# Performance work log

Hardware: AMD Instinct MI355X
Metric: run time of the kernel (lower is better)

## Reference

```python
import jax, jax.numpy as jnp
import numpy as np
from jax import lax

EPS_BN = 1e-5
EPS_LN = 1e-5
IMG = 240
BETA = 1.0

def l2norm(x, axis=-1):
    n = jnp.linalg.norm(x, axis=axis, keepdims=True)
    return x / jnp.maximum(n, 1e-12)

def bn2d(x, g, b):
    # training-mode BatchNorm2d: stats over (B,H,W), biased variance
    m = x.mean(axis=(0, 2, 3), keepdims=True)
    v = x.var(axis=(0, 2, 3), keepdims=True)
    return g[None, :, None, None] * (x - m) * lax.rsqrt(v + EPS_BN) + b[None, :, None, None]

def conv2d(x, w):
    return lax.conv_general_dilated(x, w, (1, 1), 'SAME', dimension_numbers=('NCHW', 'OIHW', 'NCHW'))

def convT2x2(x, w, b):
    # ConvTranspose2d k=2 s=2 pad=0; torch weight layout (C_in, C_out, 2, 2)
    B, C, H, W = x.shape
    O = w.shape[1]
    y = jnp.einsum('bchw,copq->bohpwq', x, w).reshape(B, O, 2 * H, 2 * W)
    return y + b[None, :, None, None]

def layernorm(x, g, b):
    m = x.mean(-1, keepdims=True)
    v = x.var(-1, keepdims=True)
    return g * (x - m) * lax.rsqrt(v + EPS_LN) + b

def setup_inputs() -> dict:
    key = jax.random.key(0)
    ks = jax.random.split(key, 12)
    L, B, K, N, D = 3, 16, 8, 256, 768
    H, MID = 128, 64
    inp = {
        'query': jax.random.normal(ks[0], (L, B, N, D), jnp.float32),
        'prompt': jax.random.normal(ks[1], (L, B, K, N, D), jnp.float32),
        'sharebn_g': jnp.ones((L, D)), 'sharebn_b': jnp.zeros((L, D)),
        'lw1': 0.02 * jax.random.normal(ks[2], (L, H, D, 3, 3)),
        'lbn1g': jnp.ones((L, H)), 'lbn1b': jnp.zeros((L, H)),
        'lwt1': 0.05 * jax.random.normal(ks[3], (L, H, H, 2, 2)), 'lbt1': jnp.zeros((L, H)),
        'lw2': 0.02 * jax.random.normal(ks[4], (L, MID, H, 3, 3)),
        'lbn2g': jnp.ones((L, MID)), 'lbn2b': jnp.zeros((L, MID)),
        'lwt2': 0.05 * jax.random.normal(ks[5], (L, MID, MID, 2, 2)), 'lbt2': jnp.zeros((L, MID)),
        'lw3': 0.05 * jax.random.normal(ks[6], (L, 2, MID, 1, 1)), 'lb3': jnp.zeros((L, 2)),
        'pool_logits': jnp.zeros((L, 2)),
        'mw1': 0.02 * jax.random.normal(ks[7], (L, H, D)),
        'mlng': jnp.ones((L, H)), 'mlnb': jnp.zeros((L, H)),
        'mw2': 0.05 * jax.random.normal(ks[8], (L, 2, H)), 'mb2': jnp.zeros((L, 2)),
    }
    return inp

def _layer(q, pf, p):
    # q: [B,N,D], pf: [B,M,D]
    B, N, D = q.shape
    g = int(N ** 0.5)
    qn = l2norm(q)
    pn = l2norm(pf)
    sim = jnp.einsum('bnc,bmc->bnm', qn, pn)              # [B,N,M]
    max_cos = sim.max(axis=-1)
    idx = sim.argmax(axis=-1)                              # [B,N]
    aligned = jnp.take_along_axis(pf, idx[:, :, None], axis=1)  # [B,N,D]
    residual = 0.5 * (1.0 - max_cos)
    an = l2norm(aligned)
    ctx = qn + BETA * jnp.abs(qn - an)                     # [B,N,D]
    cmap = ctx.transpose(0, 2, 1).reshape(B, D, g, g)
    cmap = bn2d(cmap, p['sbg'], p['sbb'])
    # local conv head
    x = jax.nn.relu(bn2d(conv2d(cmap, p['w1']), p['bn1g'], p['bn1b']))
    x = convT2x2(x, p['wt1'], p['bt1'])
    x = jax.nn.relu(bn2d(conv2d(x, p['w2']), p['bn2g'], p['bn2b']))
    x = convT2x2(x, p['wt2'], p['bt2'])
    raw = conv2d(x, p['w3']) + p['b3'][None, :, None, None]   # [B,2,4g,4g]
    # adaptive_avg_pool2d 4g -> g (exact 4x4 blocks)
    pl2c = raw.reshape(B, 2, g, 4, g, 4).mean(axis=(3, 5))    # [B,2,g,g]
    ps2c = jax.nn.softmax(pl2c, axis=1)
    patch_logits = (pl2c[:, 1] - pl2c[:, 0]).reshape(B, -1)
    patch_scores = ps2c[:, 1].reshape(B, -1)
    local_logits = jax.image.resize(raw, (B, 2, IMG, IMG), method='bilinear')
    # global head (GAP/GMP fusion over context map features)
    cf = cmap.reshape(B, D, N)
    gap = cf.mean(axis=-1)
    gmp = cf.max(axis=-1)
    pw = jax.nn.softmax(p['pl'])
    pooled = pw[0] * gap + pw[1] * gmp                     # [B,D]
    h = jax.nn.relu(layernorm(pooled @ p['mw1'].T, p['lng'], p['lnb']))
    logits2 = h @ p['mw2'].T + p['mb2']
    glogit = logits2[:, 1] - logits2[:, 0]
    return residual, patch_scores, patch_logits, glogit, local_logits, pw, idx, aligned

def reference(query, prompt, sharebn_g, sharebn_b, lw1, lbn1g, lbn1b, lwt1, lbt1,
              lw2, lbn2g, lbn2b, lwt2, lbt2, lw3, lb3, pool_logits,
              mw1, mlng, mlnb, mw2, mb2):
    L, B = query.shape[0], query.shape[1]
    outs = []
    for l in range(L):
        pf = prompt[l].reshape(B, -1, prompt.shape[-1])
        p = dict(sbg=sharebn_g[l], sbb=sharebn_b[l], w1=lw1[l], bn1g=lbn1g[l], bn1b=lbn1b[l],
                 wt1=lwt1[l], bt1=lbt1[l], w2=lw2[l], bn2g=lbn2g[l], bn2b=lbn2b[l],
                 wt2=lwt2[l], bt2=lbt2[l], w3=lw3[l], b3=lb3[l], pl=pool_logits[l],
                 mw1=mw1[l], lng=mlng[l], lnb=mlnb[l], mw2=mw2[l], mb2=mb2[l])
        outs.append(_layer(query[l], pf, p))
    stacked = tuple(jnp.stack([o[i] for o in outs]) for i in range(8))
    return stacked
```

## Files before the change

### kernel.cpp

```cpp
#include <hip/hip_runtime.h>
#include <hip/hip_bf16.h>
#include <math.h>

#define LLY 3
#define BB 16
#define NNQ 256
#define DD 768
#define MMP 2048
#define HH 128
#define MD 64
#define IMGSZ 240
#define LBTOT (LLY*BB)

#define OFF_INVQ 0
#define OFF_INVP (OFF_INVQ + LLY*BB*NNQ)
#define OFF_CMAP (OFF_INVP + LLY*BB*MMP)
#define OFF_BNSH (OFF_CMAP + LLY*BB*DD*NNQ)
#define OFF_X1   (OFF_BNSH + 2*LLY*DD)
#define OFF_BN1  (OFF_X1 + LLY*BB*HH*256)
#define OFF_T1   (OFF_BN1 + 2*LLY*HH)
#define OFF_X2   (OFF_T1 + LLY*BB*HH*1024)
#define OFF_BN2  (OFF_X2 + LLY*BB*MD*1024)
#define OFF_T2   (OFF_BN2 + 2*LLY*MD)
#define OFF_RAW3 (OFF_T2 + LLY*BB*MD*4096)
#define WS_FLOATS (OFF_RAW3 + LLY*BB*2*4096)
#define T1BSH (LBTOT*1024*HH)
#define SQH   (LBTOT*NNQ*DD)
#define OFF_C1P (OFF_T2 + 4718592)
#define OFF_C2P (OFF_T2 + 3256320)
#define OFF_PGL OFF_X1
#define X1B_SH 0
#define WT1B_SH 1600000

#define O_RES 0
#define O_PSC (O_RES + LLY*BB*NNQ)
#define O_PLG (O_PSC + LLY*BB*NNQ)
#define O_GLG (O_PLG + LLY*BB*NNQ)
#define O_LOC (O_GLG + LLY*BB)
#define O_PW  (O_LOC + LLY*BB*2*IMGSZ*IMGSZ)
#define O_IDX (O_PW + LLY*2)
#define O_ALN (O_IDX + LLY*BB*NNQ)

typedef __attribute__((ext_vector_type(8))) short bf16x8;
typedef __attribute__((ext_vector_type(4))) float f32x4;

__device__ __forceinline__ unsigned short f2bf(float f) {
    __hip_bfloat16 h = __float2bfloat16(f);
    unsigned short u;
    __builtin_memcpy(&u, &h, sizeof(u));
    return u;
}
__device__ __forceinline__ float bf2f(unsigned short h) {
    return __uint_as_float(((unsigned int)h) << 16);
}

__device__ __forceinline__ float blockReduceSum(float v, float* sm) {
    for (int o = 32; o; o >>= 1) v += __shfl_down(v, o, 64);
    __syncthreads();
    if ((threadIdx.x & 63) == 0) sm[threadIdx.x >> 6] = v;
    __syncthreads();
    return sm[0] + sm[1] + sm[2] + sm[3];
}

__global__ __launch_bounds__(192) void knormq(const float* __restrict__ query,
                                              float* __restrict__ ws) {
    __shared__ float sm[3];
    int row = blockIdx.x;
    int t = threadIdx.x;
    float4 v = *(const float4*)(query + (size_t)row * DD + t * 4);
    float ss = v.x * v.x + v.y * v.y + v.z * v.z + v.w * v.w;
    for (int o = 32; o; o >>= 1) ss += __shfl_down(ss, o, 64);
    if ((t & 63) == 0) sm[t >> 6] = ss;
    __syncthreads();
    ss = sm[0] + sm[1] + sm[2];
    float iv = 1.0f / fmaxf(sqrtf(ss), 1e-12f);
    if (t == 0) ws[OFF_INVQ + row] = iv;
    unsigned short* qh = (unsigned short*)(ws + OFF_T2);
    unsigned short* ql = qh + SQH;
    float e[4] = {v.x * iv, v.y * iv, v.z * iv, v.w * iv};
    unsigned int hp[2], lp[2];
    #pragma unroll
    for (int j = 0; j < 2; j++) {
        unsigned short h0 = f2bf(e[2*j]), h1 = f2bf(e[2*j+1]);
        unsigned short l0 = f2bf(e[2*j] - bf2f(h0)), l1 = f2bf(e[2*j+1] - bf2f(h1));
        hp[j] = (unsigned int)h0 | ((unsigned int)h1 << 16);
        lp[j] = (unsigned int)l0 | ((unsigned int)l1 << 16);
    }
    *(uint2*)(qh + (size_t)row * DD + t * 4) = make_uint2(hp[0], hp[1]);
    *(uint2*)(ql + (size_t)row * DD + t * 4) = make_uint2(lp[0], lp[1]);
}

__global__ __launch_bounds__(512) void ksimm(const float* __restrict__ prompt, float* __restrict__ ws) {
    __shared__ __align__(16) unsigned short Ah[128][40];
    __shared__ __align__(16) unsigned short Al[128][40];
    __shared__ __align__(16) unsigned short Bh[256][40];
    __shared__ __align__(16) unsigned short Bl[256][40];
    __shared__ float invL[128];
    int bid = blockIdx.x;
    int mt = bid & 15;
    int lb = bid >> 4;
    int t = threadIdx.x;
    int lane = t & 63, wave = t >> 6;
    int wm = wave >> 2, wn = wave & 3;
    int fr = lane & 15, fq = lane >> 4;
    const unsigned short* qh = (const unsigned short*)(ws + OFF_T2);
    const unsigned short* ql = qh + SQH;
    const float* pbase = prompt + (size_t)lb * MMP * DD + (size_t)(mt * 128) * DD;

    float ssq[2] = {0.f, 0.f};

    f32x4 acc[4][4];
    #pragma unroll
    for (int mi = 0; mi < 4; mi++)
        #pragma unroll
        for (int ni = 0; ni < 4; ni++) acc[mi][ni] = (f32x4){0.f, 0.f, 0.f, 0.f};

    for (int kc = 0; kc < DD; kc += 32) {
        __syncthreads();
        #pragma unroll
        for (int i = 0; i < 2; i++) {
            int f = t + i * 512;
            int row = f >> 3, c4 = f & 7;
            float4 v = *(const float4*)(pbase + (size_t)row * DD + kc + c4 * 4);
            ssq[i] += v.x * v.x + v.y * v.y + v.z * v.z + v.w * v.w;
            unsigned short h0 = f2bf(v.x), h1 = f2bf(v.y), h2 = f2bf(v.z), h3 = f2bf(v.w);
            unsigned short l0 = f2bf(v.x - bf2f(h0)), l1 = f2bf(v.y - bf2f(h1));
            unsigned short l2 = f2bf(v.z - bf2f(h2)), l3 = f2bf(v.w - bf2f(h3));
            uint2 hp = make_uint2((unsigned int)h0 | ((unsigned int)h1 << 16),
                                  (unsigned int)h2 | ((unsigned int)h3 << 16));
            uint2 lp = make_uint2((unsigned int)l0 | ((unsigned int)l1 << 16),
                                  (unsigned int)l2 | ((unsigned int)l3 << 16));
            *(uint2*)&Ah[row][c4 * 4] = hp;
            *(uint2*)&Al[row][c4 * 4] = lp;
        }
        #pragma unroll
        for (int i = 0; i < 2; i++) {
            int f = t + i * 512;
            int row = f >> 2, sg = f & 3;
            size_t go = (size_t)(lb * NNQ + row) * DD + kc + sg * 8;
            *(uint4*)&Bh[row][sg * 8] = *(const uint4*)(qh + go);
            *(uint4*)&Bl[row][sg * 8] = *(const uint4*)(ql + go);
        }
        __syncthreads();
        bf16x8 ah[4], al4[4], bh[4], bl4[4];
        #pragma unroll
        for (int mi = 0; mi < 4; mi++) {
            ah[mi]  = *(const bf16x8*)&Ah[wm * 64 + mi * 16 + fr][fq * 8];
            al4[mi] = *(const bf16x8*)&Al[wm * 64 + mi * 16 + fr][fq * 8];
        }
        #pragma unroll
        for (int ni = 0; ni < 4; ni++) {
            bh[ni]  = *(const bf16x8*)&Bh[wn * 64 + ni * 16 + fr][fq * 8];
            bl4[ni] = *(const bf16x8*)&Bl[wn * 64 + ni * 16 + fr][fq * 8];
        }
        #pragma unroll
        for (int mi = 0; mi < 4; mi++)
            #pragma unroll
            for (int ni = 0; ni < 4; ni++) {
                acc[mi][ni] = __builtin_amdgcn_mfma_f32_16x16x32_bf16(ah[mi],  bh[ni],  acc[mi][ni], 0, 0, 0);
                acc[mi][ni] = __builtin_amdgcn_mfma_f32_16x16x32_bf16(ah[mi],  bl4[ni], acc[mi][ni], 0, 0, 0);
                acc[mi][ni] = __builtin_amdgcn_mfma_f32_16x16x32_bf16(al4[mi], bh[ni],  acc[mi][ni], 0, 0, 0);
            }
    }
    #pragma unroll
    for (int i = 0; i < 2; i++) {
        float s = ssq[i];
        s += __shfl_xor(s, 1, 64);
        s += __shfl_xor(s, 2, 64);
        s += __shfl_xor(s, 4, 64);
        if ((t & 7) == 0) {
            int row = (t >> 3) + 64 * i;
            float iv = 1.0f / fmaxf(sqrtf(s), 1e-12f);
            invL[row] = iv;
            ws[OFF_INVP + lb * MMP + mt * 128 + row] = iv;
        }
    }
    __syncthreads();
    float* bestv = ws + OFF_X1;
    float* besti = ws + OFF_X1 + (size_t)LBTOT * NNQ * 32;
    #pragma unroll
    for (int ni = 0; ni < 4; ni++) {
        float bv = -1e30f; int bi = 0;
        #pragma unroll
        for (int mi = 0; mi < 4; mi++)
            #pragma unroll
            for (int rr = 0; rr < 4; rr++) {
                int lm = wm * 64 + mi * 16 + fq * 4 + rr;
                float s = acc[mi][ni][rr] * invL[lm];
                int m = mt * 128 + lm;
                if (s > bv) { bv = s; bi = m; }
            }
        #pragma unroll
        for (int o = 16; o <= 32; o <<= 1) {
            float ov = __shfl_xor(bv, o, 64);
            int oi = __shfl_xor(bi, o, 64);
            if (ov > bv || (ov == bv && oi < bi)) { bv = ov; bi = oi; }
        }
        if (fq == 0) {
            int q = wn * 64 + ni * 16 + fr;
            size_t slot = (size_t)(lb * NNQ + q) * 32 + wm * 16 + mt;
            bestv[slot] = bv;
            besti[slot] = (float)bi;
        }
    }
}

__global__ __launch_bounds__(256) void kpost(const float* __restrict__ query,
                                             const float* __restrict__ prompt,
                                             float* __restrict__ ws,
                                             float* __restrict__ out) {
    __shared__ float red_v[16];
    __shared__ int   red_i[16];
    __shared__ float Lctx[DD * 17];
    int bid = blockIdx.x;
    int nt = bid & 15;
    int lb = bid >> 4;
    int t = threadIdx.x;
    const float* bestv = ws + OFF_X1;
    const float* besti = ws + OFF_X1 + (size_t)LBTOT * NNQ * 32;
    if (t < 16) {
        int q = nt * 16 + t;
        const float* bv = bestv + (size_t)(lb * NNQ + q) * 32;
        const float* bi = besti + (size_t)(lb * NNQ + q) * 32;
        float best = -1e30f; int bidx2 = 0;
        for (int mtt = 0; mtt < 16; mtt++)
            #pragma unroll
            for (int wm = 0; wm < 2; wm++) {
                float v = bv[wm * 16 + mtt];
                if (v > best) { best = v; bidx2 = (int)bi[wm * 16 + mtt]; }
            }
        red_v[t] = best; red_i[t] = bidx2;
        out[O_RES + lb * NNQ + q] = 0.5f * (1.0f - best);
        out[O_IDX + lb * NNQ + q] = (float)bidx2;
    }
    __syncthreads();
    const float* qbase = query + (size_t)(lb * NNQ + nt * 16) * DD;
    const float* pbase = prompt + (size_t)lb * MMP * DD;
    const float* invq = ws + OFF_INVQ + lb * NNQ + nt * 16;
    const float* invp = ws + OFF_INVP + lb * MMP;
    int c = t & 15;
    int nn = t >> 4;
    int gn = nt * 16 + nn;
    int midx = red_i[nn];
    float ip = invp[midx];
    float iq = invq[nn];
    const float* prow = pbase + (size_t)midx * DD;
    const float* qrow = qbase + (size_t)nn * DD;
    float* aln = out + O_ALN + (size_t)(lb * NNQ + gn) * DD;
    for (int jj = 0; jj < DD / 16; jj++) {
        int d = c + jj * 16;
        float pvr = prow[d];
        float qv = qrow[d] * iq;
        float av = pvr * ip;
        float cx = qv + fabsf(qv - av);
        aln[d] = pvr;
        Lctx[d * 17 + nn] = cx;
    }
    __syncthreads();
    float* cm = ws + OFF_CMAP + (size_t)lb * DD * NNQ + nt * 16;
    int nl = t & 15, dd = t >> 4;
    for (int jj = 0; jj < DD / 16; jj++) {
        int d = jj * 16 + dd;
        cm[(size_t)d * NNQ + nl] = Lctx[d * 17 + nl];
    }
}

__global__ __launch_bounds__(256) void kbnstats(const float* __restrict__ x, int C, int SP,
                                                const float* __restrict__ g,
                                                const float* __restrict__ b,
                                                float* __restrict__ outSB) {
    __shared__ float sm[4];
    int bid = blockIdx.x;
    int c = bid % C;
    int l = bid / C;
    int t = threadIdx.x;
    float s = 0.f, sq = 0.f;
    for (int bb2 = 0; bb2 < BB; ++bb2) {
        const float* p = x + ((size_t)(l * BB + bb2) * C + c) * SP;
        for (int i = t; i < SP; i += 256) { float v = p[i]; s += v; sq += v * v; }
    }
    s = blockReduceSum(s, sm);
    sq = blockReduceSum(sq, sm);
    if (t == 0) {
        float inv = 1.0f / (float)(BB * SP);
        float m = s * inv;
        float var = sq * inv - m * m;
        float sc = g[l * C + c] * rsqrtf(var + 1e-5f);
        float bo = b[l * C + c] - m * sc;
        outSB[l * C + c] = sc;
        outSB[LLY * C + l * C + c] = bo;
    }
}

__global__ __launch_bounds__(256) void kw1cvt(const float* __restrict__ lw1, float* __restrict__ ws) {
    unsigned short* w1B = (unsigned short*)(ws + OFF_X2);
    int bid = blockIdx.x;
    int l = bid / HH, co = bid % HH;
    int t = threadIdx.x;
    for (int c0 = 0; c0 < DD; c0 += 256) {
        int ci = c0 + t;
        const float* src = lw1 + ((size_t)(l * HH + co) * DD + ci) * 9;
        #pragma unroll
        for (int tap = 0; tap < 9; tap++) {
            w1B[((size_t)((l * 9 + tap) * HH + co)) * DD + ci] = f2bf(src[tap]);
        }
    }
}

__global__ __launch_bounds__(256) void kbn1cvt(float* __restrict__ ws) {
    __shared__ float Ld[64][65];
    unsigned short* cmT = (unsigned short*)(ws + OFF_T2);
    int bid = blockIdx.x;
    int nt = bid & 3;
    int r = bid >> 2;
    int ct = r % 12;
    int lb = r / 12;
    int l = lb >> 4;
    int t = threadIdx.x;
    const float* cmap = ws + OFF_CMAP + (size_t)lb * DD * NNQ;
    const float* bns = ws + OFF_BNSH + l * DD;
    const float* bnb = ws + OFF_BNSH + LLY * DD + l * DD;
    #pragma unroll
    for (int i = 0; i < 4; i++) {
        int f = t + i * 256;
        int row = f >> 4, c4 = f & 15;
        int ci = ct * 64 + row;
        float4 v = *(const float4*)(cmap + (size_t)ci * NNQ + nt * 64 + c4 * 4);
        float s = bns[ci], bo = bnb[ci];
        Ld[row][c4*4+0] = v.x * s + bo; Ld[row][c4*4+1] = v.y * s + bo;
        Ld[row][c4*4+2] = v.z * s + bo; Ld[row][c4*4+3] = v.w * s + bo;
    }
    __syncthreads();
    #pragma unroll
    for (int i = 0; i < 2; i++) {
        int f = t + i * 256;
        int row = f >> 3, seg = f & 7;
        unsigned int pk[4];
        #pragma unroll
        for (int e = 0; e < 4; e++) {
            unsigned int lo = f2bf(Ld[seg * 8 + 2 * e][row]);
            unsigned int hi = f2bf(Ld[seg * 8 + 2 * e + 1][row]);
            pk[e] = lo | (hi << 16);
        }
        uint4 o = make_uint4(pk[0], pk[1], pk[2], pk[3]);
        *(uint4*)(cmT + ((size_t)(lb * NNQ + nt * 64 + row)) * DD + ct * 64 + seg * 8) = o;
    }
}

__global__ __launch_bounds__(256) void kconv1m(float* __restrict__ ws) {
    __shared__ __align__(16) unsigned short Ab[128][72];
    __shared__ __align__(16) unsigned short Bb[128][72];
    int bid = blockIdx.x;
    int s = bid % 6;
    int ntile = (bid / 6) & 1;
    int lb = bid / 12;
    int l = lb >> 4;
    int t = threadIdx.x;
    int lane = t & 63;
    int wave = t >> 6;
    int wr = wave >> 1, wc = wave & 1;
    int fr = lane & 15, fq = lane >> 4;
    const unsigned short* w1B = (const unsigned short*)(ws + OFF_X2);
    const unsigned short* cmT = (const unsigned short*)(ws + OFF_T2);

    f32x4 acc[4][4];
    #pragma unroll
    for (int mi = 0; mi < 4; mi++)
        #pragma unroll
        for (int ni = 0; ni < 4; ni++) acc[mi][ni] = (f32x4){0.f, 0.f, 0.f, 0.f};

    for (int g = s * 18; g < s * 18 + 18; ++g) {
        int tap = g / 12;
        int kc = (g % 12) * 64;
        int dy = tap / 3 - 1, dx = tap % 3 - 1;
        const unsigned short* wpl = w1B + (size_t)((l * 9 + tap) * HH) * DD;
        __syncthreads();
        #pragma unroll
        for (int i = 0; i < 4; i++) {
            int f = t + i * 256;
            int row = f >> 3, seg = f & 7;
            uint4 v = *(const uint4*)(wpl + (size_t)row * DD + kc + seg * 8);
            *(uint4*)&Ab[row][seg * 8] = v;
        }
        #pragma unroll
        for (int i = 0; i < 4; i++) {
            int f = t + i * 256;
            int row = f >> 3, seg = f & 7;
            int n = ntile * 128 + row;
            int y = (n >> 4) + dy, x = (n & 15) + dx;
            bool ok = ((unsigned)y < 16u) && ((unsigned)x < 16u);
            uint4 v = make_uint4(0u, 0u, 0u, 0u);
            if (ok) v = *(const uint4*)(cmT + ((size_t)(lb * NNQ + y * 16 + x)) * DD + kc + seg * 8);
            *(uint4*)&Bb[row][seg * 8] = v;
        }
        __syncthreads();
        #pragma unroll
        for (int kk = 0; kk < 64; kk += 32) {
            bf16x8 af[4], bfv[4];
            #pragma unroll
            for (int mi = 0; mi < 4; mi++)
                af[mi] = *(const bf16x8*)&Ab[wr * 64 + mi * 16 + fr][kk + fq * 8];
            #pragma unroll
            for (int ni = 0; ni < 4; ni++)
                bfv[ni] = *(const bf16x8*)&Bb[wc * 64 + ni * 16 + fr][kk + fq * 8];
            #pragma unroll
            for (int mi = 0; mi < 4; mi++)
                #pragma unroll
                for (int ni = 0; ni < 4; ni++)
                    acc[mi][ni] = __builtin_amdgcn_mfma_f32_16x16x32_bf16(af[mi], bfv[ni], acc[mi][ni], 0, 0, 0);
        }
    }
    float* dst = (s == 5) ? (ws + OFF_X1 + (size_t)lb * HH * 256)
                          : (ws + OFF_C1P + (size_t)(s * LBTOT + lb) * (HH * 256));
    #pragma unroll
    for (int mi = 0; mi < 4; mi++) {
        #pragma unroll
        for (int ni = 0; ni < 4; ni++) {
            int gn = ntile * 128 + wc * 64 + ni * 16 + fr;
            #pragma unroll
            for (int rr = 0; rr < 4; rr++) {
                int co = wr * 64 + mi * 16 + fq * 4 + rr;
                dst[(size_t)co * 256 + gn] = acc[mi][ni][rr];
            }
        }
    }
}

__global__ __launch_bounds__(256) void kc1red(float* __restrict__ ws) {
    size_t i = ((size_t)blockIdx.x * 256 + threadIdx.x) * 8;
    float4 a0 = *(float4*)(ws + OFF_X1 + i);
    float4 a1 = *(float4*)(ws + OFF_X1 + i + 4);
    #pragma unroll
    for (int s = 0; s < 5; s++) {
        const float* p = ws + OFF_C1P + (size_t)s * (LBTOT * HH * 256) + i;
        float4 b0 = *(const float4*)p;
        float4 b1 = *(const float4*)(p + 4);
        a0.x += b0.x; a0.y += b0.y; a0.z += b0.z; a0.w += b0.w;
        a1.x += b1.x; a1.y += b1.y; a1.z += b1.z; a1.w += b1.w;
    }
    *(float4*)(ws + OFF_X1 + i) = a0;
    *(float4*)(ws + OFF_X1 + i + 4) = a1;
}

__global__ __launch_bounds__(256) void kxcvt(const float* __restrict__ x,
                                             const float* __restrict__ sbsb,
                                             unsigned short* __restrict__ xb,
                                             int CI, int SPIN, int nT, int cT) {
    __shared__ float Ld[64][65];
    int bid = blockIdx.x;
    int nt = bid % nT;
    int r = bid / nT;
    int ct = r % cT;
    int lb = r / cT;
    int l = lb >> 4;
    int t = threadIdx.x;
    const float* sc = sbsb + l * CI;
    const float* bo = sbsb + LLY * CI + l * CI;
    #pragma unroll
    for (int i = 0; i < 4; i++) {
        int f = t + i * 256;
        int row = f >> 4, c4 = f & 15;
        int ci = ct * 64 + row;
        float4 v = *(const float4*)(x + ((size_t)lb * CI + ci) * SPIN + nt * 64 + c4 * 4);
        float s = sc[ci], b_ = bo[ci];
        Ld[row][c4*4+0] = fmaxf(v.x * s + b_, 0.f);
        Ld[row][c4*4+1] = fmaxf(v.y * s + b_, 0.f);
        Ld[row][c4*4+2] = fmaxf(v.z * s + b_, 0.f);
        Ld[row][c4*4+3] = fmaxf(v.w * s + b_, 0.f);
    }
    __syncthreads();
    int segs = CI >> 3;
    for (int f = t; f < 64 * segs; f += 256) {
        int row = f / segs, seg = f % segs;
        int sl = seg - ct * 8;
        if (sl < 0 || sl >= 8) continue;
        unsigned int pk[4];
        #pragma unroll
        for (int e = 0; e < 4; e++) {
            unsigned int lo = f2bf(Ld[sl * 8 + 2 * e][row]);
            unsigned int hi = f2bf(Ld[sl * 8 + 2 * e + 1][row]);
            pk[e] = lo | (hi << 16);
        }
        uint4 o = make_uint4(pk[0], pk[1], pk[2], pk[3]);
        *(uint4*)(xb + ((size_t)lb * SPIN + nt * 64 + row) * CI + ct * 64 + sl * 8) = o;
    }
}

__global__ __launch_bounds__(128) void kwtcvt(const float* __restrict__ lwt,
                                              unsigned short* __restrict__ dst,
                                              int CI, int CO) {
    int bid = blockIdx.x;
    int l = bid / CO, co = bid % CO;
    int t = threadIdx.x;
    if (t < CI) {
        const float* src = lwt + (((size_t)(l * CI + t) * CO + co) * 4);
        #pragma unroll
        for (int pq = 0; pq < 4; pq++) {
            dst[((size_t)((l * 4 + pq) * CO + co)) * CI + t] = f2bf(src[pq]);
        }
    }
}

__global__ __launch_bounds__(256) void kconvTm(const unsigned short* __restrict__ xb,
                                               const unsigned short* __restrict__ wtb,
                                               const float* __restrict__ bt,
                                               float* __restrict__ xout,
                                               int CI, int CO, int gsh, int nTiles, int coTiles) {
    __shared__ __align__(16) unsigned short Ab[64][72];
    __shared__ __align__(16) unsigned short Bb[256][72];
    int bid = blockIdx.x;
    int ntile = bid % nTiles;
    int r = bid / nTiles;
    int cot = r % coTiles; r /= coTiles;
    int pq = r & 3;
    int lb = r >> 2;
    int l = lb >> 4;
    int SPIN = 1 << (2 * gsh);
    int t = threadIdx.x, lane = t & 63, wave = t >> 6;
    int fr = lane & 15, fq = lane >> 4;

    f32x4 acc[4][4];
    #pragma unroll
    for (int mi = 0; mi < 4; mi++)
        #pragma unroll
        for (int ni = 0; ni < 4; ni++) acc[mi][ni] = (f32x4){0.f, 0.f, 0.f, 0.f};

    for (int kc = 0; kc < CI; kc += 64) {
        __syncthreads();
        #pragma unroll
        for (int i = 0; i < 2; i++) {
            int f = t + i * 256;
            int row = f >> 3, seg = f & 7;
            *(uint4*)&Ab[row][seg * 8] =
                *(const uint4*)(wtb + ((size_t)((l * 4 + pq) * CO + cot * 64 + row)) * CI + kc + seg * 8);
        }
        #pragma unroll
        for (int i = 0; i < 8; i++) {
            int f = t + i * 256;
            int row = f >> 3, seg = f & 7;
            *(uint4*)&Bb[row][seg * 8] =
                *(const uint4*)(xb + ((size_t)lb * SPIN + ntile * 256 + row) * CI + kc + seg * 8);
        }
        __syncthreads();
        #pragma unroll
        for (int kk = 0; kk < 64; kk += 32) {
            bf16x8 af[4], bfv[4];
            #pragma unroll
            for (int mi = 0; mi < 4; mi++)
                af[mi] = *(const bf16x8*)&Ab[mi * 16 + fr][kk + fq * 8];
            #pragma unroll
            for (int ni = 0; ni < 4; ni++)
                bfv[ni] = *(const bf16x8*)&Bb[wave * 64 + ni * 16 + fr][kk + fq * 8];
            #pragma unroll
            for (int mi = 0; mi < 4; mi++)
                #pragma unroll
                for (int ni = 0; ni < 4; ni++)
                    acc[mi][ni] = __builtin_amdgcn_mfma_f32_16x16x32_bf16(af[mi], bfv[ni], acc[mi][ni], 0, 0, 0);
        }
    }
    int p = pq >> 1, q = pq & 1;
    int GIN = 1 << gsh;
    #pragma unroll
    for (int mi = 0; mi < 4; mi++) {
        #pragma unroll
        for (int rr = 0; rr < 4; rr++) {
            int co = cot * 64 + mi * 16 + fq * 4 + rr;
            float bias = bt[l * CO + co];
            float* orow = xout + ((size_t)(lb * CO + co)) * (4 * SPIN);
            #pragma unroll
            for (int ni = 0; ni < 4; ni++) {
                int n = ntile * 256 + wave * 64 + ni * 16 + fr;
                int h = n >> gsh, w = n & (GIN - 1);
                orow[(2 * h + p) * (2 * GIN) + 2 * w + q] = acc[mi][ni][rr] + bias;
            }
        }
    }
}

__global__ __launch_bounds__(256) void kconvT2f(const unsigned short* __restrict__ xb,
                                                const unsigned short* __restrict__ wtb,
                                                const float* __restrict__ bt,
                                                const float* __restrict__ lw3,
                                                const float* __restrict__ lb3,
                                                float* __restrict__ ws) {
    __shared__ __align__(16) unsigned short Ab[64][72];
    __shared__ __align__(16) unsigned short Bb[256][72];
    __shared__ float w3s[2][64];
    int bid = blockIdx.x;
    int ntile = bid & 3;
    int r = bid >> 2;
    int pq = r & 3;
    int lb = r >> 2;
    int l = lb >> 4;
    const int CI = MD, CO = MD, gsh = 5;
    int SPIN = 1 << (2 * gsh);
    int t = threadIdx.x, lane = t & 63, wave = t >> 6;
    int fr = lane & 15, fq = lane >> 4;
    if (t < 128) w3s[t >> 6][t & 63] = lw3[(size_t)(l * 2 + (t >> 6)) * MD + (t & 63)];

    f32x4 acc[4][4];
    #pragma unroll
    for (int mi = 0; mi < 4; mi++)
        #pragma unroll
        for (int ni = 0; ni < 4; ni++) acc[mi][ni] = (f32x4){0.f, 0.f, 0.f, 0.f};

    __syncthreads();
    #pragma unroll
    for (int i = 0; i < 2; i++) {
        int f = t + i * 256;
        int row = f >> 3, seg = f & 7;
        *(uint4*)&Ab[row][seg * 8] =
            *(const uint4*)(wtb + ((size_t)((l * 4 + pq) * CO + row)) * CI + seg * 8);
    }
    #pragma unroll
    for (int i = 0; i < 8; i++) {
        int f = t + i * 256;
        int row = f >> 3, seg = f & 7;
        *(uint4*)&Bb[row][seg * 8] =
            *(const uint4*)(xb + ((size_t)lb * SPIN + ntile * 256 + row) * CI + seg * 8);
    }
    __syncthreads();
    #pragma unroll
    for (int kk = 0; kk < 64; kk += 32) {
        bf16x8 af[4], bfv[4];
        #pragma unroll
        for (int mi = 0; mi < 4; mi++)
            af[mi] = *(const bf16x8*)&Ab[mi * 16 + fr][kk + fq * 8];
        #pragma unroll
        for (int ni = 0; ni < 4; ni++)
            bfv[ni] = *(const bf16x8*)&Bb[wave * 64 + ni * 16 + fr][kk + fq * 8];
        #pragma unroll
        for (int mi = 0; mi < 4; mi++)
            #pragma unroll
            for (int ni = 0; ni < 4; ni++)
                acc[mi][ni] = __builtin_amdgcn_mfma_f32_16x16x32_bf16(af[mi], bfv[ni], acc[mi][ni], 0, 0, 0);
    }
    float s0[4] = {0.f, 0.f, 0.f, 0.f};
    float s1[4] = {0.f, 0.f, 0.f, 0.f};
    #pragma unroll
    for (int mi = 0; mi < 4; mi++) {
        #pragma unroll
        for (int rr = 0; rr < 4; rr++) {
            int co = mi * 16 + fq * 4 + rr;
            float bias = bt[l * CO + co];
            float w0 = w3s[0][co], w1 = w3s[1][co];
            #pragma unroll
            for (int ni = 0; ni < 4; ni++) {
                float val = acc[mi][ni][rr] + bias;
                s0[ni] += w0 * val;
                s1[ni] += w1 * val;
            }
        }
    }
    #pragma unroll
    for (int ni = 0; ni < 4; ni++) {
        s0[ni] += __shfl_xor(s0[ni], 16, 64); s0[ni] += __shfl_xor(s0[ni], 32, 64);
        s1[ni] += __shfl_xor(s1[ni], 16, 64); s1[ni] += __shfl_xor(s1[ni], 32, 64);
    }
    if (fq == 0) {
        int p = pq >> 1, q = pq & 1;
        float* r3 = ws + OFF_RAW3 + (size_t)lb * 2 * 4096;
        float b30 = lb3[l * 2], b31 = lb3[l * 2 + 1];
        #pragma unroll
        for (int ni = 0; ni < 4; ni++) {
            int n = ntile * 256 + wave * 64 + ni * 16 + fr;
            int h = n >> 5, w = n & 31;
            int opix = (2 * h + p) * 64 + 2 * w + q;
            r3[opix] = s0[ni] + b30;
            r3[4096 + opix] = s1[ni] + b31;
        }
    }
}

__global__ __launch_bounds__(256) void kt1cvt(float* __restrict__ ws) {
    __shared__ float Ld[64][65];
    unsigned short* t1B = (unsigned short*)(ws + OFF_T2);
    int bid = blockIdx.x;
    int ntile = bid & 15;
    int r = bid >> 4;
    int ct = r & 1;
    int lb = r >> 1;
    int t = threadIdx.x;
    const float* t1p = ws + OFF_T1 + (size_t)lb * HH * 1024;
    #pragma unroll
    for (int i = 0; i < 4; i++) {
        int f = t + i * 256;
        int row = f >> 4, c4 = f & 15;
        float4 v = *(const float4*)(t1p + (size_t)(ct * 64 + row) * 1024 + ntile * 64 + c4 * 4);
        *(float4*)&Ld[row][c4 * 4] = v;
    }
    __syncthreads();
    #pragma unroll
    for (int i = 0; i < 2; i++) {
        int f = t + i * 256;
        int row = f >> 3, seg = f & 7;
        unsigned int pk[4];
        #pragma unroll
        for (int e = 0; e < 4; e++) {
            unsigned int lo = f2bf(Ld[seg * 8 + 2 * e][row]);
            unsigned int hi = f2bf(Ld[seg * 8 + 2 * e + 1][row]);
            pk[e] = lo | (hi << 16);
        }
        uint4 o = make_uint4(pk[0], pk[1], pk[2], pk[3]);
        *(uint4*)(t1B + ((size_t)(lb * 1024 + ntile * 64 + row)) * HH + ct * 64 + seg * 8) = o;
    }
}

__global__ __launch_bounds__(256) void kw2cvt(const float* __restrict__ lw2, float* __restrict__ ws) {
    unsigned short* w2B = (unsigned short*)(ws + OFF_T2) + T1BSH;
    int bid = blockIdx.x;
    int l = bid / MD, co = bid % MD;
    int t = threadIdx.x;
    if (t < HH) {
        int ci = t;
        const float* src = lw2 + ((size_t)(l * MD + co) * HH + ci) * 9;
        #pragma unroll
        for (int tap = 0; tap < 9; tap++) {
            w2B[((size_t)((l * 9 + tap) * MD + co)) * HH + ci] = f2bf(src[tap]);
        }
    }
}

__global__ __launch_bounds__(256) void kconv2m(float* __restrict__ ws) {
    __shared__ __align__(16) unsigned short Ab[64][72];
    __shared__ __align__(16) unsigned short Bb[256][72];
    int bid = blockIdx.x;
    int s = bid & 1;
    int ntile = (bid >> 1) & 3;
    int lb = bid >> 3;
    int l = lb >> 4;
    int t = threadIdx.x;
    int lane = t & 63;
    int wave = t >> 6;
    int fr = lane & 15, fq = lane >> 4;
    const unsigned short* t1B = (const unsigned short*)(ws + OFF_T2);
    const unsigned short* w2B = (const unsigned short*)(ws + OFF_T2) + T1BSH;

    f32x4 acc[4][4];
    #pragma unroll
    for (int mi = 0; mi < 4; mi++)
        #pragma unroll
        for (int ni = 0; ni < 4; ni++) acc[mi][ni] = (f32x4){0.f, 0.f, 0.f, 0.f};

    for (int g = s * 9; g < s * 9 + 9; ++g) {
        int tap = g >> 1;
        int kc = (g & 1) * 64;
        int dy = tap / 3 - 1, dx = tap % 3 - 1;
        const unsigned short* wpl = w2B + (size_t)((l * 9 + tap) * MD) * HH;
        __syncthreads();
        #pragma unroll
        for (int i = 0; i < 2; i++) {
            int f = t + i * 256;
            int row = f >> 3, seg = f & 7;
            uint4 v = *(const uint4*)(wpl + (size_t)row * HH + kc + seg * 8);
            *(uint4*)&Ab[row][seg * 8] = v;
        }
        #pragma unroll
        for (int i = 0; i < 8; i++) {
            int f = t + i * 256;
            int row = f >> 3, seg = f & 7;
            int n = ntile * 256 + row;
            int y = (n >> 5) + dy, x = (n & 31) + dx;
            bool ok = ((unsigned)y < 32u) && ((unsigned)x < 32u);
            uint4 v = make_uint4(0u, 0u, 0u, 0u);
            if (ok) v = *(const uint4*)(t1B + ((size_t)(lb * 1024 + y * 32 + x)) * HH + kc + seg * 8);
            *(uint4*)&Bb[row][seg * 8] = v;
        }
        __syncthreads();
        #pragma unroll
        for (int kk = 0; kk < 64; kk += 32) {
            bf16x8 af[4], bfv[4];
            #pragma unroll
            for (int mi = 0; mi < 4; mi++)
                af[mi] = *(const bf16x8*)&Ab[mi * 16 + fr][kk + fq * 8];
            #pragma unroll
            for (int ni = 0; ni < 4; ni++)
                bfv[ni] = *(const bf16x8*)&Bb[wave * 64 + ni * 16 + fr][kk + fq * 8];
            #pragma unroll
            for (int mi = 0; mi < 4; mi++)
                #pragma unroll
                for (int ni = 0; ni < 4; ni++)
                    acc[mi][ni] = __builtin_amdgcn_mfma_f32_16x16x32_bf16(af[mi], bfv[ni], acc[mi][ni], 0, 0, 0);
        }
    }
    float* dst = (s == 1) ? (ws + OFF_X2 + (size_t)lb * MD * 1024)
                          : (ws + OFF_C2P + (size_t)lb * MD * 1024);
    #pragma unroll
    for (int mi = 0; mi < 4; mi++) {
        #pragma unroll
        for (int ni = 0; ni < 4; ni++) {
            int gn = ntile * 256 + wave * 64 + ni * 16 + fr;
            #pragma unroll
            for (int rr = 0; rr < 4; rr++) {
                int co = mi * 16 + fq * 4 + rr;
                dst[(size_t)co * 1024 + gn] = acc[mi][ni][rr];
            }
        }
    }
}

__global__ __launch_bounds__(256) void kc2red(float* __restrict__ ws) {
    size_t i = ((size_t)blockIdx.x * 256 + threadIdx.x) * 8;
    float4 a0 = *(float4*)(ws + OFF_X2 + i);
    float4 a1 = *(float4*)(ws + OFF_X2 + i + 4);
    const float* p = ws + OFF_C2P + i;
    float4 b0 = *(const float4*)p;
    float4 b1 = *(const float4*)(p + 4);
    a0.x += b0.x; a0.y += b0.y; a0.z += b0.z; a0.w += b0.w;
    a1.x += b1.x; a1.y += b1.y; a1.z += b1.z; a1.w += b1.w;
    *(float4*)(ws + OFF_X2 + i) = a0;
    *(float4*)(ws + OFF_X2 + i + 4) = a1;
}

__global__ __launch_bounds__(256) void kpool(const float* __restrict__ ws, float* __restrict__ out) {
    int lb = blockIdx.x;
    int t = threadIdx.x;
    int gy = t >> 4, gx = t & 15;
    const float* r3 = ws + OFF_RAW3 + (size_t)lb * 2 * 4096;
    float pl[2];
    #pragma unroll
    for (int ch = 0; ch < 2; ch++) {
        const float* basep = r3 + ch * 4096;
        float s = 0.f;
        #pragma unroll
        for (int dy = 0; dy < 4; dy++)
            #pragma unroll
            for (int dx = 0; dx < 4; dx++)
                s += basep[(gy * 4 + dy) * 64 + gx * 4 + dx];
        pl[ch] = s * (1.f / 16.f);
    }
    out[O_PLG + lb * NNQ + t] = pl[1] - pl[0];
    out[O_PSC + lb * NNQ + t] = 1.f / (1.f + expf(pl[0] - pl[1]));
}

__global__ __launch_bounds__(256) void kresize(const float* __restrict__ ws, float* __restrict__ out) {
    int id = blockIdx.x * 256 + threadIdx.x;
    int ox = id % IMGSZ;
    int tmp = id / IMGSZ;
    int oy = tmp % IMGSZ;
    int tmp2 = tmp / IMGSZ;
    int ch = tmp2 & 1;
    int lb = tmp2 >> 1;
    const float S = 64.f / 240.f;
    float xs = fminf(fmaxf((ox + 0.5f) * S - 0.5f, 0.f), 63.f);
    float ys = fminf(fmaxf((oy + 0.5f) * S - 0.5f, 0.f), 63.f);
    int x0 = (int)xs, y0 = (int)ys;
    float fx = xs - x0, fy = ys - y0;
    int x1 = min(x0 + 1, 63), y1 = min(y0 + 1, 63);
    const float* basep = ws + OFF_RAW3 + (size_t)(lb * 2 + ch) * 4096;
    float v00 = basep[y0 * 64 + x0], v01 = basep[y0 * 64 + x1];
    float v10 = basep[y1 * 64 + x0], v11 = basep[y1 * 64 + x1];
    float v = (1.f - fy) * ((1.f - fx) * v00 + fx * v01) + fy * ((1.f - fx) * v10 + fx * v11);
    out[O_LOC + id] = v;
}

__global__ __launch_bounds__(256) void kgap(float* __restrict__ ws,
                                            const float* __restrict__ pool_logits) {
    int bid = blockIdx.x;
    int dchunk = bid % 12;
    int lb = bid / 12;
    int l = lb >> 4;
    int t = threadIdx.x;
    int r = t >> 2, p = t & 3;
    int d = dchunk * 64 + r;
    const float* row = ws + OFF_CMAP + (size_t)lb * DD * NNQ + (size_t)d * NNQ + p * 64;
    float s = 0.f, mx = -1e30f, mn = 1e30f;
    #pragma unroll
    for (int i = 0; i < 16; i++) {
        float4 v = *(const float4*)(row + i * 4);
        s += v.x + v.y + v.z + v.w;
        mx = fmaxf(mx, fmaxf(fmaxf(v.x, v.y), fmaxf(v.z, v.w)));
        mn = fminf(mn, fminf(fminf(v.x, v.y), fminf(v.z, v.w)));
    }
    s += __shfl_xor(s, 1, 64); s += __shfl_xor(s, 2, 64);
    mx = fmaxf(mx, __shfl_xor(mx, 1, 64)); mx = fmaxf(mx, __shfl_xor(mx, 2, 64));
    mn = fminf(mn, __shfl_xor(mn, 1, 64)); mn = fminf(mn, __shfl_xor(mn, 2, 64));
    if (p == 0) {
        float p0 = pool_logits[l * 2], p1 = pool_logits[l * 2 + 1];
        float mxp = fmaxf(p0, p1);
        float e0 = expf(p0 - mxp), e1 = expf(p1 - mxp);
        float pw0 = e0 / (e0 + e1), pw1 = e1 / (e0 + e1);
        const float* bns = ws + OFF_BNSH + l * DD;
        const float* bnb = ws + OFF_BNSH + LLY * DD + l * DD;
        float scv = bns[d], bov = bnb[d];
        float gap = scv * (s * (1.f / NNQ)) + bov;
        float gmp = (scv >= 0.f) ? (scv * mx + bov) : (scv * mn + bov);
        ws[OFF_PGL + lb * DD + d] = pw0 * gap + pw1 * gmp;
    }
}

__global__ __launch_bounds__(256) void kglob2(const float* __restrict__ ws,
                                              const float* __restrict__ pool_logits,
                                              const float* __restrict__ mw1,
                                              const float* __restrict__ mlng,
                                              const float* __restrict__ mlnb,
                                              const float* __restrict__ mw2,
                                              const float* __restrict__ mb2,
                                              float* __restrict__ out) {
    __shared__ float pooled[DD];
    __shared__ float zbuf[HH];
    __shared__ float hbuf[HH];
    __shared__ float sm[4];
    int lb = blockIdx.x;
    int l = lb >> 4;
    int b = lb & 15;
    int t = threadIdx.x;
    float p0 = pool_logits[l * 2], p1 = pool_logits[l * 2 + 1];
    float mx = fmaxf(p0, p1);
    float e0 = expf(p0 - mx), e1 = expf(p1 - mx);
    float pw0 = e0 / (e0 + e1), pw1 = e1 / (e0 + e1);
    if (b == 0 && t < 2) out[O_PW + l * 2 + t] = (t == 0) ? pw0 : pw1;

    for (int d = t; d < DD; d += 256) pooled[d] = ws[OFF_PGL + lb * DD + d];
    __syncthreads();
    if (t < HH) {
        const float* wrow = mw1 + (size_t)(l * HH + t) * DD;
        float a = 0.f;
        for (int d2 = 0; d2 < DD; d2++) a += pooled[d2] * wrow[d2];
        zbuf[t] = a;
    }
    __syncthreads();
    float zv = (t < HH) ? zbuf[t] : 0.f;
    float s1r = blockReduceSum(zv, sm);
    float s2r = blockReduceSum(zv * zv, sm);
    float mean = s1r * (1.f / HH);
    float var = s2r * (1.f / HH) - mean * mean;
    float rstd = rsqrtf(var + 1e-5f);
    if (t < HH) {
        float h = (zbuf[t] - mean) * rstd * mlng[l * HH + t] + mlnb[l * HH + t];
        hbuf[t] = fmaxf(h, 0.f);
    }
    __syncthreads();
    float hv = (t < HH) ? hbuf[t] : 0.f;
    float w0v = (t < HH) ? mw2[(size_t)(l * 2 + 0) * HH + t] : 0.f;
    float w1v = (t < HH) ? mw2[(size_t)(l * 2 + 1) * HH + t] : 0.f;
    float s0 = blockReduceSum(hv * w0v, sm);
    float s1 = blockReduceSum(hv * w1v, sm);
    if (t == 0) out[O_GLG + lb] = (s1 + mb2[l * 2 + 1]) - (s0 + mb2[l * 2]);
}

extern "C" void kernel_launch(void* const* d_in, const int* in_sizes, int n_in,
                              void* d_out, int out_size, void* d_ws, size_t ws_size,
                              hipStream_t stream) {
    const float* query      = (const float*)d_in[0];
    const float* prompt     = (const float*)d_in[1];
    const float* sharebn_g  = (const float*)d_in[2];
    const float* sharebn_b  = (const float*)d_in[3];
    const float* lw1        = (const float*)d_in[4];
    const float* lbn1g      = (const float*)d_in[5];
    const float* lbn1b      = (const float*)d_in[6];
    const float* lwt1       = (const float*)d_in[7];
    const float* lbt1       = (const float*)d_in[8];
    const float* lw2        = (const float*)d_in[9];
    const float* lbn2g      = (const float*)d_in[10];
    const float* lbn2b      = (const float*)d_in[11];
    const float* lwt2       = (const float*)d_in[12];
    const float* lbt2       = (const float*)d_in[13];
    const float* lw3        = (const float*)d_in[14];
    const float* lb3        = (const float*)d_in[15];
    const float* pool_logits= (const float*)d_in[16];
    const float* mw1        = (const float*)d_in[17];
    const float* mlng       = (const float*)d_in[18];
    const float* mlnb       = (const float*)d_in[19];
    const float* mw2        = (const float*)d_in[20];
    const float* mb2        = (const float*)d_in[21];
    float* out = (float*)d_out;
    float* ws = (float*)d_ws;

    hipLaunchKernelGGL(knormq, dim3(LLY*BB*NNQ), dim3(192), 0, stream, query, ws);
    hipLaunchKernelGGL(ksimm, dim3(LBTOT*16), dim3(512), 0, stream, prompt, ws);
    hipLaunchKernelGGL(kpost, dim3(LBTOT*16), dim3(256), 0, stream, query, prompt, ws, out);
    hipLaunchKernelGGL(kbnstats, dim3(LLY*DD), dim3(256), 0, stream,
                       ws + OFF_CMAP, DD, NNQ, sharebn_g, sharebn_b, ws + OFF_BNSH);
    hipLaunchKernelGGL(kw1cvt, dim3(LLY*HH), dim3(256), 0, stream, lw1, ws);
    hipLaunchKernelGGL(kbn1cvt, dim3(LBTOT*48), dim3(256), 0, stream, ws);
    hipLaunchKernelGGL(kconv1m, dim3(LBTOT*12), dim3(256), 0, stream, ws);
    hipLaunchKernelGGL(kc1red, dim3(768), dim3(256), 0, stream, ws);
    hipLaunchKernelGGL(kbnstats, dim3(LLY*HH), dim3(256), 0, stream,
                       ws + OFF_X1, HH, 256, lbn1g, lbn1b, ws + OFF_BN1);
    hipLaunchKernelGGL(kxcvt, dim3(LBTOT*8), dim3(256), 0, stream,
                       ws + OFF_X1, ws + OFF_BN1, (unsigned short*)(ws + OFF_T2) + X1B_SH,
                       HH, 256, 4, 2);
    hipLaunchKernelGGL(kwtcvt, dim3(LLY*HH), dim3(128), 0, stream,
                       lwt1, (unsigned short*)(ws + OFF_T2) + WT1B_SH, HH, HH);
    hipLaunchKernelGGL(kconvTm, dim3(LBTOT*4*2), dim3(256), 0, stream,
                       (const unsigned short*)(ws + OFF_T2) + X1B_SH,
                       (const unsigned short*)(ws + OFF_T2) + WT1B_SH,
                       lbt1, ws + OFF_T1, HH, HH, 4, 1, 2);
    hipLaunchKernelGGL(kt1cvt, dim3(LBTOT*32), dim3(256), 0, stream, ws);
    hipLaunchKernelGGL(kw2cvt, dim3(LLY*MD), dim3(256), 0, stream, lw2, ws);
    hipLaunchKernelGGL(kconv2m, dim3(LBTOT*8), dim3(256), 0, stream, ws);
    hipLaunchKernelGGL(kc2red, dim3(1536), dim3(256), 0, stream, ws);
    hipLaunchKernelGGL(kbnstats, dim3(LLY*MD), dim3(256), 0, stream,
                       ws + OFF_X2, MD, 1024, lbn2g, lbn2b, ws + OFF_BN2);
    hipLaunchKernelGGL(kxcvt, dim3(LBTOT*16), dim3(256), 0, stream,
                       ws + OFF_X2, ws + OFF_BN2, (unsigned short*)(ws + OFF_X1),
                       MD, 1024, 16, 1);
    hipLaunchKernelGGL(kwtcvt, dim3(LLY*MD), dim3(128), 0, stream,
                       lwt2, (unsigned short*)(ws + OFF_X2), MD, MD);
    hipLaunchKernelGGL(kconvT2f, dim3(LBTOT*4*4), dim3(256), 0, stream,
                       (const unsigned short*)(ws + OFF_X1),
                       (const unsigned short*)(ws + OFF_X2),
                       lbt2, lw3, lb3, ws);
    hipLaunchKernelGGL(kpool, dim3(LBTOT), dim3(256), 0, stream, ws, out);
    hipLaunchKernelGGL(kresize, dim3(LLY*BB*2*IMGSZ*IMGSZ/256), dim3(256), 0, stream, ws, out);
    hipLaunchKernelGGL(kgap, dim3(LBTOT*12), dim3(256), 0, stream, ws, pool_logits);
    hipLaunchKernelGGL(kglob2, dim3(LBTOT), dim3(256), 0, stream,
                       ws, pool_logits, mw1, mlng, mlnb, mw2, mb2, out);
}
```

Measured before the change: 490.0 us.

## Fuse shared-BN and pooling partial stats into kpost epilogue

kpost now writes per-tile partial sums, sums of squares, maxes and mins per channel from its shared-memory tile. New small kernels reduce these partials into BN scale/shift (kbnfin) and the pooled GAP/GMP vector (kgapf). This replaces two full re-reads of the 37M-float context map (kbnstats and kgap). It moves the pooled buffer to offset 0 in the workspace, adds a partial-stats buffer in the C1P region, and computes variance as E[x²]−m², which can lose precision.

Result: no change. 494.0 us (+0.8%).

```diff
diff --git a/kernel.cpp b/kernel.cpp
--- a/kernel.cpp
+++ b/kernel.cpp
@@ -28,7 +28,7 @@
 #define SQH   (LBTOT*NNQ*DD)
 #define OFF_C1P (OFF_T2 + 4718592)
 #define OFF_C2P (OFF_T2 + 3256320)
-#define OFF_PGL OFF_X1
+#define OFF_PGL 0
 #define X1B_SH 0
 #define WT1B_SH 1600000
 
@@ -263,6 +263,79 @@
         int d = jj * 16 + dd;
         cm[(size_t)d * NNQ + nl] = Lctx[d * 17 + nl];
     }
+    {
+        float* pp = ws + OFF_C1P + (size_t)(lb * 16 + nt) * (DD * 4);
+        #pragma unroll
+        for (int k = 0; k < 3; k++) {
+            int d = t * 3 + k;
+            float s = 0.f, sq = 0.f, mx = -1e30f, mn = 1e30f;
+            #pragma unroll
+            for (int n2 = 0; n2 < 16; n2++) {
+                float v = Lctx[d * 17 + n2];
+                s += v; sq += v * v;
+                mx = fmaxf(mx, v); mn = fminf(mn, v);
+            }
+            pp[d] = s;
+            pp[DD + d] = sq;
+            pp[2 * DD + d] = mx;
+            pp[3 * DD + d] = mn;
+        }
+    }
+}
+
+__global__ __launch_bounds__(256) void kbnfin(const float* __restrict__ g,
+                                              const float* __restrict__ b,
+                                              float* __restrict__ ws) {
+    __shared__ float ssm[4][64], sqm[4][64];
+    int chunk = blockIdx.x % 12;
+    int l = blockIdx.x / 12;
+    int t = threadIdx.x;
+    int d = chunk * 64 + (t & 63);
+    int r = t >> 6;
+    float s = 0.f, sq = 0.f;
+    for (int j = r; j < 256; j += 4) {
+        const float* pp = ws + OFF_C1P + (size_t)(l * 256 + j) * (DD * 4);
+        s += pp[d];
+        sq += pp[DD + d];
+    }
+    ssm[r][t & 63] = s; sqm[r][t & 63] = sq;
+    __syncthreads();
+    if (r == 0) {
+        s  = ssm[0][t] + ssm[1][t] + ssm[2][t] + ssm[3][t];
+        sq = sqm[0][t] + sqm[1][t] + sqm[2][t] + sqm[3][t];
+        float inv = 1.0f / 4096.f;
+        float m = s * inv;
+        float var = sq * inv - m * m;
+        float sc = g[l * DD + d] * rsqrtf(var + 1e-5f);
+        float bo = b[l * DD + d] - m * sc;
+        ws[OFF_BNSH + l * DD + d] = sc;
+        ws[OFF_BNSH + LLY * DD + l * DD + d] = bo;
+    }
+}
+
+__global__ __launch_bounds__(64) void kgapf(float* __restrict__ ws,
+                                            const float* __restrict__ pool_logits) {
+    int chunk = blockIdx.x % 12;
+    int lb = blockIdx.x / 12;
+    int l = lb >> 4;
+    int t = threadIdx.x;
+    int d = chunk * 64 + t;
+    float s = 0.f, mx = -1e30f, mn = 1e30f;
+    for (int nt = 0; nt < 16; nt++) {
+        const float* pp = ws + OFF_C1P + (size_t)(lb * 16 + nt) * (DD * 4);
+        s += pp[d];
+        mx = fmaxf(mx, pp[2 * DD + d]);
+        mn = fminf(mn, pp[3 * DD + d]);
+    }
+    float p0 = pool_logits[l * 2], p1 = pool_logits[l * 2 + 1];
+    float mxp = fmaxf(p0, p1);
+    float e0 = expf(p0 - mxp), e1 = expf(p1 - mxp);
+    float pw0 = e0 / (e0 + e1), pw1 = e1 / (e0 + e1);
+    float sc = ws[OFF_BNSH + l * DD + d];
+    float bo = ws[OFF_BNSH + LLY * DD + l * DD + d];
+    float gap = sc * (s * (1.f / NNQ)) + bo;
+    float gmp = (sc >= 0.f) ? (sc * mx + bo) : (sc * mn + bo);
+    ws[OFF_PGL + lb * DD + d] = pw0 * gap + pw1 * gmp;
 }
 
 __global__ __launch_bounds__(256) void kbnstats(const float* __restrict__ x, int C, int SP,
@@ -852,41 +925,6 @@
     float v10 = basep[y1 * 64 + x0], v11 = basep[y1 * 64 + x1];
     float v = (1.f - fy) * ((1.f - fx) * v00 + fx * v01) + fy * ((1.f - fx) * v10 + fx * v11);
     out[O_LOC + id] = v;
-}
-
-__global__ __launch_bounds__(256) void kgap(float* __restrict__ ws,
-                                            const float* __restrict__ pool_logits) {
-    int bid = blockIdx.x;
-    int dchunk = bid % 12;
-    int lb = bid / 12;
-    int l = lb >> 4;
-    int t = threadIdx.x;
-    int r = t >> 2, p = t & 3;
-    int d = dchunk * 64 + r;
-    const float* row = ws + OFF_CMAP + (size_t)lb * DD * NNQ + (size_t)d * NNQ + p * 64;
-    float s = 0.f, mx = -1e30f, mn = 1e30f;
-    #pragma unroll
-    for (int i = 0; i < 16; i++) {
-        float4 v = *(const float4*)(row + i * 4);
-        s += v.x + v.y + v.z + v.w;
-        mx = fmaxf(mx, fmaxf(fmaxf(v.x, v.y), fmaxf(v.z, v.w)));
-        mn = fminf(mn, fminf(fminf(v.x, v.y), fminf(v.z, v.w)));
-    }
-    s += __shfl_xor(s, 1, 64); s += __shfl_xor(s, 2, 64);
-    mx = fmaxf(mx, __shfl_xor(mx, 1, 64)); mx = fmaxf(mx, __shfl_xor(mx, 2, 64));
-    mn = fminf(mn, __shfl_xor(mn, 1, 64)); mn = fminf(mn, __shfl_xor(mn, 2, 64));
-    if (p == 0) {
-        float p0 = pool_logits[l * 2], p1 = pool_logits[l * 2 + 1];
-        float mxp = fmaxf(p0, p1);
-        float e0 = expf(p0 - mxp), e1 = expf(p1 - mxp);
-        float pw0 = e0 / (e0 + e1), pw1 = e1 / (e0 + e1);
-        const float* bns = ws + OFF_BNSH + l * DD;
-        const float* bnb = ws + OFF_BNSH + LLY * DD + l * DD;
-        float scv = bns[d], bov = bnb[d];
-        float gap = scv * (s * (1.f / NNQ)) + bov;
-        float gmp = (scv >= 0.f) ? (scv * mx + bov) : (scv * mn + bov);
-        ws[OFF_PGL + lb * DD + d] = pw0 * gap + pw1 * gmp;
-    }
 }
 
 __global__ __launch_bounds__(256) void kglob2(const float* __restrict__ ws,
@@ -970,8 +1008,8 @@
     hipLaunchKernelGGL(knormq, dim3(LLY*BB*NNQ), dim3(192), 0, stream, query, ws);
     hipLaunchKernelGGL(ksimm, dim3(LBTOT*16), dim3(512), 0, stream, prompt, ws);
     hipLaunchKernelGGL(kpost, dim3(LBTOT*16), dim3(256), 0, stream, query, prompt, ws, out);
-    hipLaunchKernelGGL(kbnstats, dim3(LLY*DD), dim3(256), 0, stream,
-                       ws + OFF_CMAP, DD, NNQ, sharebn_g, sharebn_b, ws + OFF_BNSH);
+    hipLaunchKernelGGL(kbnfin, dim3(LLY*12), dim3(256), 0, stream, sharebn_g, sharebn_b, ws);
+    hipLaunchKernelGGL(kgapf, dim3(LBTOT*12), dim3(64), 0, stream, ws, pool_logits);
     hipLaunchKernelGGL(kw1cvt, dim3(LLY*HH), dim3(256), 0, stream, lw1, ws);
     hipLaunchKernelGGL(kbn1cvt, dim3(LBTOT*48), dim3(256), 0, stream, ws);
     hipLaunchKernelGGL(kconv1m, dim3(LBTOT*12), dim3(256), 0, stream, ws);
@@ -1004,7 +1042,6 @@
                        lbt2, lw3, lb3, ws);
     hipLaunchKernelGGL(kpool, dim3(LBTOT), dim3(256), 0, stream, ws, out);
     hipLaunchKernelGGL(kresize, dim3(LLY*BB*2*IMGSZ*IMGSZ/256), dim3(256), 0, stream, ws, out);
-    hipLaunchKernelGGL(kgap, dim3(LBTOT*12), dim3(256), 0, stream, ws, pool_logits);
     hipLaunchKernelGGL(kglob2, dim3(LBTOT), dim3(256), 0, stream,
                        ws, pool_logits, mw1, mlng, mlnb, mw2, mb2, out);
 }
```
